# Kernel tuning notes

Measured on AMD Instinct MI355X. Metric: run time of the kernel, lower is better.

The kernel has to match this reference:

```python
import jax, jax.numpy as jnp
import numpy as np

B, S, D = 8, 2048, 768

def setup_inputs() -> dict:
    key = jax.random.key(0)
    k1, k2, k3, k4 = jax.random.split(key, 4)
    scale = 1.0 / np.sqrt(D)
    x = jax.random.normal(k1, (B, S, D), dtype=jnp.float32)
    W = jax.random.normal(k2, (D, D), dtype=jnp.float32) * scale
    proj_w = jax.random.normal(k3, (D, D), dtype=jnp.float32) * scale
    proj_b = jax.random.normal(k4, (D,), dtype=jnp.float32) * scale
    return {"x": x, "W": W, "proj_w": proj_w, "proj_b": proj_b}


def reference(x, W, proj_w, proj_b):
    # Wx = Linear(x) with torch convention: x @ W.T  -> [B,S,D]
    Wx = jnp.einsum('bsd,ed->bse', x, W)
    # s = Wx @ x^T  -> [B,S,S]
    s = jnp.einsum('bse,bte->bst', Wx, x)
    # mask diagonal (self) with -inf
    eye = jnp.eye(S, dtype=bool)
    s = jnp.where(eye[None, :, :], -jnp.inf, s)
    a = jax.nn.softmax(s, axis=2)
    # c = a @ x -> [B,S,D]
    c = jnp.einsum('bst,btd->bsd', a, x)
    # proj + relu, residual; dropout with p=0 is identity
    c = jax.nn.relu(jnp.einsum('bsd,ed->bse', c, proj_w) + proj_b)
    return x + c
```

## Files before the change

kernel.cpp:

```cpp
#include <hip/hip_runtime.h>
#include <hip/hip_bf16.h>

typedef _Float16 fp16_t;
typedef __attribute__((ext_vector_type(8))) _Float16 fp16x8;
typedef __attribute__((ext_vector_type(4))) _Float16 fp16x4;
typedef __attribute__((ext_vector_type(4))) float fx4;

#define GLDS(g, l)                                                              \
  __builtin_amdgcn_global_load_lds(                                             \
      (const __attribute__((address_space(1))) void*)(g),                       \
      (__attribute__((address_space(3))) void*)(l), 16, 0, 0)

enum { EPI_F32 = 0, EPI_F16 = 1, EPI_FUSE = 2, EPI_SOFT = 3 };

__device__ __forceinline__ void xcd_decode(int& bx, int& by, int& bz) {
  const int nx = gridDim.x, ny = gridDim.y;
  const int lid = (int)(blockIdx.x + nx * (blockIdx.y + ny * blockIdx.z));
  const int j = lid & 7, k = lid >> 3;
  bx = k % nx;
  const int s = j + 8 * (k / nx);
  by = s % ny;
  bz = s / ny;
}

template <bool ASPLIT, int EPI>
__global__ __launch_bounds__(256) void gemm_bt(
    const fp16_t* __restrict__ A1, const fp16_t* __restrict__ A2,
    const fp16_t* __restrict__ B1, void* __restrict__ Cv, int K, int lda,
    int ldb, long long sA, long long sB, long long sC,
    const float* __restrict__ bias, const float* __restrict__ resid,
    float* __restrict__ m_out, float* __restrict__ l_out) {
  constexpr int ALO = ASPLIT ? 128 * 32 : 0;
  __shared__ __align__(16) fp16_t As[128 * 32 + ALO];
  __shared__ __align__(16) fp16_t Bs[128 * 32];
  __shared__ float sred[(EPI == EPI_SOFT) ? 256 : 1];
  __shared__ float sfin[(EPI == EPI_SOFT) ? 128 : 1];

  const int tid  = threadIdx.x;
  const int lane = tid & 63;
  const int w    = tid >> 6;
  const int wr   = w >> 1;
  const int wc   = w & 1;

  int bx, by, bz;
  xcd_decode(bx, by, bz);
  const int N = (int)gridDim.x * 128;
  const long long tile_m = (long long)by * 128;
  const long long tile_n = (long long)bx * 128;
  const long long z = bz;
  const long long aoff = z * sA + tile_m * (long long)lda;
  const long long boff = z * sB + tile_n * (long long)ldb;

  fx4 acc[4][4];
#pragma unroll
  for (int i = 0; i < 4; i++)
#pragma unroll
    for (int j = 0; j < 4; j++) acc[i][j] = (fx4){0.f, 0.f, 0.f, 0.f};

  const int r_l = lane >> 2;
  const int c_l = ((((lane & 3) + ((r_l >> 1) & 3)) & 3) << 3);
  const int frow = lane & 15;
  const int qoff = (((lane >> 4) - ((frow >> 1) & 3)) & 3) << 3;

  const size_t sa0 = (size_t)(w * 16 + r_l) * lda + c_l;
  const size_t sa1 = (size_t)(64 + w * 16 + r_l) * lda + c_l;
  const size_t sb0 = (size_t)(w * 16 + r_l) * ldb + c_l;
  const size_t sb1 = (size_t)(64 + w * 16 + r_l) * ldb + c_l;
  const int ld0 = (w * 16) * 32;
  const int ld1 = (64 + w * 16) * 32;

  for (int kt = 0; kt < K; kt += 32) {
    __syncthreads();
    {
      const fp16_t* gah = A1 + aoff + kt;
      const fp16_t* gbh = B1 + boff + kt;
      GLDS(gah + sa0, &As[ld0]);
      GLDS(gah + sa1, &As[ld1]);
      GLDS(gbh + sb0, &Bs[ld0]);
      GLDS(gbh + sb1, &Bs[ld1]);
      if (ASPLIT) {
        const fp16_t* gal = A2 + aoff + kt;
        GLDS(gal + sa0, &As[ALO + ld0]);
        GLDS(gal + sa1, &As[ALO + ld1]);
      }
    }
    __syncthreads();

    fp16x8 afh[4], bbh[4], afl[4];
#pragma unroll
    for (int mi = 0; mi < 4; mi++)
      afh[mi] = *(const fp16x8*)&As[(wr * 64 + mi * 16 + frow) * 32 + qoff];
#pragma unroll
    for (int ni = 0; ni < 4; ni++)
      bbh[ni] = *(const fp16x8*)&Bs[(wc * 64 + ni * 16 + frow) * 32 + qoff];
    if (ASPLIT) {
#pragma unroll
      for (int mi = 0; mi < 4; mi++)
        afl[mi] =
            *(const fp16x8*)&As[ALO + (wr * 64 + mi * 16 + frow) * 32 + qoff];
    }

#pragma unroll
    for (int mi = 0; mi < 4; mi++)
#pragma unroll
      for (int ni = 0; ni < 4; ni++) {
        fx4 a = acc[mi][ni];
        a = __builtin_amdgcn_mfma_f32_16x16x32_f16(afh[mi], bbh[ni], a, 0, 0, 0);
        if (ASPLIT)
          a = __builtin_amdgcn_mfma_f32_16x16x32_f16(afl[mi], bbh[ni], a, 0, 0, 0);
        acc[mi][ni] = a;
      }
  }

  const int er = (lane >> 4) * 4;
  const int ec = lane & 15;
  const long long crow = tile_m + wr * 64;
  const long long ccol = tile_n + wc * 64;

  if constexpr (EPI == EPI_SOFT) {
    float pm[4][4];
#pragma unroll
    for (int mi = 0; mi < 4; mi++)
#pragma unroll
      for (int j = 0; j < 4; j++) {
        const long long r = crow + mi * 16 + er + j;
        float mx = -1e30f;
#pragma unroll
        for (int ni = 0; ni < 4; ni++) {
          const long long cc = ccol + ni * 16 + ec;
          float v = acc[mi][ni][j];
          if (r == cc) v = -1e30f;
          acc[mi][ni][j] = v;
          mx = fmaxf(mx, v);
        }
        pm[mi][j] = mx;
      }
#pragma unroll
    for (int o = 1; o < 16; o <<= 1)
#pragma unroll
      for (int mi = 0; mi < 4; mi++)
#pragma unroll
        for (int j = 0; j < 4; j++)
          pm[mi][j] = fmaxf(pm[mi][j], __shfl_xor(pm[mi][j], o, 64));
    if (ec == 0) {
#pragma unroll
      for (int mi = 0; mi < 4; mi++)
#pragma unroll
        for (int j = 0; j < 4; j++)
          sred[wc * 128 + wr * 64 + mi * 16 + er + j] = pm[mi][j];
    }
    __syncthreads();
    if (tid < 128) sfin[tid] = fmaxf(sred[tid], sred[128 + tid]);
    __syncthreads();
    float ps[4][4];
#pragma unroll
    for (int mi = 0; mi < 4; mi++)
#pragma unroll
      for (int j = 0; j < 4; j++) {
        const float m = sfin[wr * 64 + mi * 16 + er + j];
        float s = 0.f;
#pragma unroll
        for (int ni = 0; ni < 4; ni++) {
          const float e = __expf(acc[mi][ni][j] - m);
          acc[mi][ni][j] = e;
          s += e;
        }
        ps[mi][j] = s;
      }
#pragma unroll
    for (int o = 1; o < 16; o <<= 1)
#pragma unroll
      for (int mi = 0; mi < 4; mi++)
#pragma unroll
        for (int j = 0; j < 4; j++)
          ps[mi][j] += __shfl_xor(ps[mi][j], o, 64);
    __syncthreads();
    if (ec == 0) {
#pragma unroll
      for (int mi = 0; mi < 4; mi++)
#pragma unroll
        for (int j = 0; j < 4; j++)
          sred[wc * 128 + wr * 64 + mi * 16 + er + j] = ps[mi][j];
    }
    __syncthreads();
    if (tid < 128) {
      const long long si = (z * 16 + bx) * 2048 + tile_m + tid;
      m_out[si] = sfin[tid];
      l_out[si] = sred[tid] + sred[128 + tid];
    }
#pragma unroll
    for (int mi = 0; mi < 4; mi++)
#pragma unroll
      for (int j = 0; j < 4; j++) {
        const long long r = crow + mi * 16 + er + j;
#pragma unroll
        for (int ni = 0; ni < 4; ni++) {
          const long long cc = ccol + ni * 16 + ec;
          ((fp16_t*)Cv)[z * sC + r * N + cc] = (fp16_t)acc[mi][ni][j];
        }
      }
  } else {
#pragma unroll
    for (int mi = 0; mi < 4; mi++)
#pragma unroll
      for (int j = 0; j < 4; j++) {
        const long long r = crow + mi * 16 + er + j;
#pragma unroll
        for (int ni = 0; ni < 4; ni++) {
          const long long cc = ccol + ni * 16 + ec;
          const long long idx = z * sC + r * N + cc;
          const float v = acc[mi][ni][j];
          if (EPI == EPI_F32) {
            ((float*)Cv)[idx] = v;
          } else if (EPI == EPI_F16) {
            ((fp16_t*)Cv)[idx] = (fp16_t)v;
          } else {
            float u = v + bias[cc];
            u = u > 0.f ? u : 0.f;
            ((float*)Cv)[idx] = resid[r * N + cc] + u;
          }
        }
      }
  }
}

__global__ __launch_bounds__(256) void softmerge(
    const float* __restrict__ mstat, const float* __restrict__ lstat,
    float* __restrict__ scale) {
  const int gr = blockIdx.x * 256 + threadIdx.x;
  const int z = gr >> 11, row = gr & 2047;
  const long long base = ((long long)z * 16) * 2048 + row;
  float mv[16], lv[16];
  float m = -1e30f;
#pragma unroll
  for (int t = 0; t < 16; t++) {
    mv[t] = mstat[base + t * 2048];
    m = fmaxf(m, mv[t]);
  }
  float l = 0.f;
#pragma unroll
  for (int t = 0; t < 16; t++) {
    lv[t] = lstat[base + t * 2048];
    l += lv[t] * __expf(mv[t] - m);
  }
  const float il = 1.0f / l;
#pragma unroll
  for (int t = 0; t < 16; t++) scale[base + t * 2048] = __expf(mv[t] - m) * il;
}

__global__ __launch_bounds__(256) void gemm_pv(
    const fp16_t* __restrict__ P, const float* __restrict__ scale,
    const fp16_t* __restrict__ Bx, fp16_t* __restrict__ C) {
  __shared__ __align__(16) fp16_t As[128 * 32];
  __shared__ __align__(16) fp16_t Bs[128 * 32];

  const int tid  = threadIdx.x;
  const int lane = tid & 63;
  const int w    = tid >> 6;
  const int wr   = w >> 1;
  const int wc   = w & 1;

  int bx, by, bz;
  xcd_decode(bx, by, bz);
  const long long tile_m = (long long)by * 128;
  const long long tile_n = (long long)bx * 128;
  const long long z = bz;

  fx4 acc[4][4];
#pragma unroll
  for (int i = 0; i < 4; i++)
#pragma unroll
    for (int j = 0; j < 4; j++) acc[i][j] = (fx4){0.f, 0.f, 0.f, 0.f};

  const int r_l = lane >> 2;
  const int c_l = ((((lane & 3) + ((r_l >> 1) & 3)) & 3) << 3);
  const int frow = lane & 15;
  const int qoff = (((lane >> 4) - ((frow >> 1) & 3)) & 3) << 3;
  const size_t sb0 = (size_t)(w * 16 + r_l) * 2048 + c_l;
  const size_t sb1 = (size_t)(64 + w * 16 + r_l) * 2048 + c_l;
  const int ld0 = (w * 16) * 32;
  const int ld1 = (64 + w * 16) * 32;
  const fp16_t* B = Bx + z * (768LL * 2048) + tile_n * 2048;

  const int r = tid >> 1, hh = tid & 1;
  const int gm = (int)tile_m + r;
  const fp16_t* prow = P + z * (2048LL * 2048) + (long long)gm * 2048 + hh * 16;
  const float* srow = scale + (long long)z * 16 * 2048 + gm;
  const int slot0 = ((2 * hh + 0) - ((r >> 1) & 3)) & 3;
  const int slot1 = ((2 * hh + 1) - ((r >> 1) & 3)) & 3;
  fp16_t* const wp0 = &As[r * 32 + slot0 * 8];
  fp16_t* const wp1 = &As[r * 32 + slot1 * 8];

  for (int kt0 = 0; kt0 < 2048; kt0 += 128) {
    const fp16_t sh = (fp16_t)srow[(kt0 >> 7) * 2048];
#pragma unroll
    for (int ki = 0; ki < 4; ki++) {
      const int kt = kt0 + ki * 32;
      fp16x8 c0 = *(const fp16x8*)(prow + kt);
      fp16x8 c1 = *(const fp16x8*)(prow + kt + 8);
      c0 *= sh;
      c1 *= sh;
      __syncthreads();
      *(fp16x8*)wp0 = c0;
      *(fp16x8*)wp1 = c1;
      GLDS(B + kt + sb0, &Bs[ld0]);
      GLDS(B + kt + sb1, &Bs[ld1]);
      __syncthreads();

      fp16x8 af[4], bb[4];
#pragma unroll
      for (int mi = 0; mi < 4; mi++)
        af[mi] = *(const fp16x8*)&As[(wr * 64 + mi * 16 + frow) * 32 + qoff];
#pragma unroll
      for (int ni = 0; ni < 4; ni++)
        bb[ni] = *(const fp16x8*)&Bs[(wc * 64 + ni * 16 + frow) * 32 + qoff];
#pragma unroll
      for (int mi = 0; mi < 4; mi++)
#pragma unroll
        for (int ni = 0; ni < 4; ni++)
          acc[mi][ni] = __builtin_amdgcn_mfma_f32_16x16x32_f16(
              af[mi], bb[ni], acc[mi][ni], 0, 0, 0);
    }
  }

  const int er = (lane >> 4) * 4;
  const int ec = lane & 15;
  const long long crow = tile_m + wr * 64;
  const long long ccol = tile_n + wc * 64;
  fp16_t* Cz = C + z * (2048LL * 768);
#pragma unroll
  for (int mi = 0; mi < 4; mi++)
#pragma unroll
    for (int j = 0; j < 4; j++) {
      const long long rr = crow + mi * 16 + er + j;
#pragma unroll
      for (int ni = 0; ni < 4; ni++)
        Cz[rr * 768 + ccol + ni * 16 + ec] = (fp16_t)acc[mi][ni][j];
    }
}

__global__ __launch_bounds__(256) void prep_x(
    const float* __restrict__ x, fp16_t* __restrict__ xh,
    fp16_t* __restrict__ xl, fp16_t* __restrict__ xT) {
  __shared__ fp16_t t[32][33];
  const int b = blockIdx.z;
  const int d0 = blockIdx.x * 32;
  const int s0 = blockIdx.y * 32;
  const float* ib = x + (long long)b * 2048 * 768;
  const int tx = threadIdx.x & 31;
  const int ty = threadIdx.x >> 5;
#pragma unroll
  for (int i = 0; i < 4; i++) {
    const int srow = s0 + ty + i * 8;
    const long long idx = (long long)b * 2048 * 768 + (long long)srow * 768 + d0 + tx;
    const float v = ib[(long long)srow * 768 + d0 + tx];
    const fp16_t h = (fp16_t)v;
    xh[idx] = h;
    xl[idx] = (fp16_t)(v - (float)h);
    t[ty + i * 8][tx] = h;
  }
  __syncthreads();
#pragma unroll
  for (int i = 0; i < 4; i++)
    xT[(long long)b * 768 * 2048 + (long long)(d0 + ty + i * 8) * 2048 + s0 + tx] =
        t[tx][ty + i * 8];
}

__global__ __launch_bounds__(256) void cast_f32_f16(
    const float* __restrict__ in, fp16_t* __restrict__ out, int n4) {
  const int i = blockIdx.x * 256 + threadIdx.x;
  if (i >= n4) return;
  const float4 v = ((const float4*)in)[i];
  ((fp16x4*)out)[i] =
      (fp16x4){(fp16_t)v.x, (fp16_t)v.y, (fp16_t)v.z, (fp16_t)v.w};
}

extern "C" void kernel_launch(void* const* d_in, const int* in_sizes, int n_in,
                              void* d_out, int out_size, void* d_ws,
                              size_t ws_size, hipStream_t stream) {
  const float* x  = (const float*)d_in[0];
  const float* W  = (const float*)d_in[1];
  const float* pw = (const float*)d_in[2];
  const float* pb = (const float*)d_in[3];

  const long long S = 2048, D = 768;
  const long long BS = 8 * S;

  char* p = (char*)d_ws;
  auto carve = [&](long long bytes) {
    char* q = p;
    p += (bytes + 255) & ~255LL;
    return q;
  };
  fp16_t* xh = (fp16_t*)carve(BS * D * 2);
  fp16_t* xl = (fp16_t*)carve(BS * D * 2);
  fp16_t* xT = (fp16_t*)carve(BS * D * 2);
  fp16_t* Wx = (fp16_t*)carve(BS * D * 2);
  fp16_t* Wh = (fp16_t*)carve(D * D * 2);
  fp16_t* ph = (fp16_t*)carve(D * D * 2);
  float*  mstat = (float*)carve(BS * 16 * 4);
  float*  lstat = (float*)carve(BS * 16 * 4);
  float*  scale = (float*)carve(BS * 16 * 4);
  fp16_t* Ps = (fp16_t*)carve(8 * S * S * 2);
  fp16_t* cb = Wx;

  prep_x<<<dim3(24, 64, 8), 256, 0, stream>>>(x, xh, xl, xT);
  cast_f32_f16<<<(unsigned)(D * D / 4 / 256), 256, 0, stream>>>(
      W, Wh, (int)(D * D / 4));
  cast_f32_f16<<<(unsigned)(D * D / 4 / 256), 256, 0, stream>>>(
      pw, ph, (int)(D * D / 4));

  gemm_bt<true, EPI_F16><<<dim3(6, 128, 1), 256, 0, stream>>>(
      xh, xl, Wh, Wx, 768, 768, 768, 0, 0, 0, nullptr, nullptr, nullptr,
      nullptr);

  gemm_bt<false, EPI_SOFT><<<dim3(16, 16, 8), 256, 0, stream>>>(
      Wx, nullptr, xh, Ps, 768, 768, 768, S * D, S * D, S * S, nullptr,
      nullptr, mstat, lstat);

  softmerge<<<(unsigned)(BS / 256), 256, 0, stream>>>(mstat, lstat, scale);

  gemm_pv<<<dim3(6, 16, 8), 256, 0, stream>>>(Ps, scale, xT, cb);

  gemm_bt<false, EPI_FUSE><<<dim3(6, 128, 1), 256, 0, stream>>>(
      cb, nullptr, ph, (float*)d_out, 768, 768, 768, 0, 0, 0, pb, x, nullptr,
      nullptr);
}
```

Baseline: 404.4 us.

## Fuse softmax merge into PV gemm, double K step, merge weight casts

Removes the separate softmerge kernel by computing the per-tile softmax rescale factors inside gemm_pv's prologue, and merges the two weight-cast kernels into a single launch. Both GEMM kernels now stage 64 K-elements per barrier pair (two 32-wide LDS buffers) instead of 32, which halves the number of syncs. The softmax epilogue is also simplified: per-row shuffle reductions, one fewer barrier, and the exp values are written out directly. The aim is fewer launches and less synchronisation, at the cost of more LDS per block and redundant scale recomputation across the column blocks of gemm_pv.

```diff
diff --git a/kernel.cpp b/kernel.cpp
--- a/kernel.cpp
+++ b/kernel.cpp
@@ -31,10 +31,10 @@
     const float* __restrict__ bias, const float* __restrict__ resid,
     float* __restrict__ m_out, float* __restrict__ l_out) {
   constexpr int ALO = ASPLIT ? 128 * 32 : 0;
-  __shared__ __align__(16) fp16_t As[128 * 32 + ALO];
-  __shared__ __align__(16) fp16_t Bs[128 * 32];
-  __shared__ float sred[(EPI == EPI_SOFT) ? 256 : 1];
-  __shared__ float sfin[(EPI == EPI_SOFT) ? 128 : 1];
+  __shared__ __align__(16) fp16_t As[2][128 * 32 + ALO];
+  __shared__ __align__(16) fp16_t Bs[2][128 * 32];
+  __shared__ float smax[(EPI == EPI_SOFT) ? 256 : 1];
+  __shared__ float ssum[(EPI == EPI_SOFT) ? 256 : 1];
 
   const int tid  = threadIdx.x;
   const int lane = tid & 63;
@@ -69,47 +69,50 @@
   const int ld0 = (w * 16) * 32;
   const int ld1 = (64 + w * 16) * 32;
 
-  for (int kt = 0; kt < K; kt += 32) {
+  for (int kt = 0; kt < K; kt += 64) {
     __syncthreads();
-    {
-      const fp16_t* gah = A1 + aoff + kt;
-      const fp16_t* gbh = B1 + boff + kt;
-      GLDS(gah + sa0, &As[ld0]);
-      GLDS(gah + sa1, &As[ld1]);
-      GLDS(gbh + sb0, &Bs[ld0]);
-      GLDS(gbh + sb1, &Bs[ld1]);
+#pragma unroll
+    for (int h = 0; h < 2; h++) {
+      const fp16_t* gah = A1 + aoff + kt + h * 32;
+      const fp16_t* gbh = B1 + boff + kt + h * 32;
+      GLDS(gah + sa0, &As[h][ld0]);
+      GLDS(gah + sa1, &As[h][ld1]);
+      GLDS(gbh + sb0, &Bs[h][ld0]);
+      GLDS(gbh + sb1, &Bs[h][ld1]);
       if (ASPLIT) {
-        const fp16_t* gal = A2 + aoff + kt;
-        GLDS(gal + sa0, &As[ALO + ld0]);
-        GLDS(gal + sa1, &As[ALO + ld1]);
+        const fp16_t* gal = A2 + aoff + kt + h * 32;
+        GLDS(gal + sa0, &As[h][ALO + ld0]);
+        GLDS(gal + sa1, &As[h][ALO + ld1]);
       }
     }
     __syncthreads();
 
-    fp16x8 afh[4], bbh[4], afl[4];
-#pragma unroll
-    for (int mi = 0; mi < 4; mi++)
-      afh[mi] = *(const fp16x8*)&As[(wr * 64 + mi * 16 + frow) * 32 + qoff];
-#pragma unroll
-    for (int ni = 0; ni < 4; ni++)
-      bbh[ni] = *(const fp16x8*)&Bs[(wc * 64 + ni * 16 + frow) * 32 + qoff];
-    if (ASPLIT) {
+#pragma unroll
+    for (int h = 0; h < 2; h++) {
+      fp16x8 afh[4], bbh[4], afl[4];
 #pragma unroll
       for (int mi = 0; mi < 4; mi++)
-        afl[mi] =
-            *(const fp16x8*)&As[ALO + (wr * 64 + mi * 16 + frow) * 32 + qoff];
-    }
-
-#pragma unroll
-    for (int mi = 0; mi < 4; mi++)
-#pragma unroll
-      for (int ni = 0; ni < 4; ni++) {
-        fx4 a = acc[mi][ni];
-        a = __builtin_amdgcn_mfma_f32_16x16x32_f16(afh[mi], bbh[ni], a, 0, 0, 0);
-        if (ASPLIT)
-          a = __builtin_amdgcn_mfma_f32_16x16x32_f16(afl[mi], bbh[ni], a, 0, 0, 0);
-        acc[mi][ni] = a;
-      }
+        afh[mi] = *(const fp16x8*)&As[h][(wr * 64 + mi * 16 + frow) * 32 + qoff];
+#pragma unroll
+      for (int ni = 0; ni < 4; ni++)
+        bbh[ni] = *(const fp16x8*)&Bs[h][(wc * 64 + ni * 16 + frow) * 32 + qoff];
+      if (ASPLIT) {
+#pragma unroll
+        for (int mi = 0; mi < 4; mi++)
+          afl[mi] =
+              *(const fp16x8*)&As[h][ALO + (wr * 64 + mi * 16 + frow) * 32 + qoff];
+      }
+#pragma unroll
+      for (int mi = 0; mi < 4; mi++)
+#pragma unroll
+        for (int ni = 0; ni < 4; ni++) {
+          fx4 a = acc[mi][ni];
+          a = __builtin_amdgcn_mfma_f32_16x16x32_f16(afh[mi], bbh[ni], a, 0, 0, 0);
+          if (ASPLIT)
+            a = __builtin_amdgcn_mfma_f32_16x16x32_f16(afl[mi], bbh[ni], a, 0, 0, 0);
+          acc[mi][ni] = a;
+        }
+    }
   }
 
   const int er = (lane >> 4) * 4;
@@ -118,7 +121,6 @@
   const long long ccol = tile_n + wc * 64;
 
   if constexpr (EPI == EPI_SOFT) {
-    float pm[4][4];
 #pragma unroll
     for (int mi = 0; mi < 4; mi++)
 #pragma unroll
@@ -133,72 +135,35 @@
           acc[mi][ni][j] = v;
           mx = fmaxf(mx, v);
         }
-        pm[mi][j] = mx;
-      }
-#pragma unroll
-    for (int o = 1; o < 16; o <<= 1)
-#pragma unroll
-      for (int mi = 0; mi < 4; mi++)
-#pragma unroll
-        for (int j = 0; j < 4; j++)
-          pm[mi][j] = fmaxf(pm[mi][j], __shfl_xor(pm[mi][j], o, 64));
-    if (ec == 0) {
-#pragma unroll
-      for (int mi = 0; mi < 4; mi++)
-#pragma unroll
-        for (int j = 0; j < 4; j++)
-          sred[wc * 128 + wr * 64 + mi * 16 + er + j] = pm[mi][j];
-    }
+#pragma unroll
+        for (int o = 1; o < 16; o <<= 1) mx = fmaxf(mx, __shfl_xor(mx, o, 64));
+        if (ec == 0) smax[wc * 128 + wr * 64 + mi * 16 + er + j] = mx;
+      }
     __syncthreads();
-    if (tid < 128) sfin[tid] = fmaxf(sred[tid], sred[128 + tid]);
-    __syncthreads();
-    float ps[4][4];
 #pragma unroll
     for (int mi = 0; mi < 4; mi++)
 #pragma unroll
       for (int j = 0; j < 4; j++) {
-        const float m = sfin[wr * 64 + mi * 16 + er + j];
+        const int rid = wr * 64 + mi * 16 + er + j;
+        const float m = fmaxf(smax[rid], smax[128 + rid]);
+        const long long r = crow + mi * 16 + er + j;
         float s = 0.f;
 #pragma unroll
         for (int ni = 0; ni < 4; ni++) {
           const float e = __expf(acc[mi][ni][j] - m);
-          acc[mi][ni][j] = e;
           s += e;
+          ((fp16_t*)Cv)[z * sC + r * N + (ccol + ni * 16 + ec)] = (fp16_t)e;
         }
-        ps[mi][j] = s;
-      }
-#pragma unroll
-    for (int o = 1; o < 16; o <<= 1)
-#pragma unroll
-      for (int mi = 0; mi < 4; mi++)
-#pragma unroll
-        for (int j = 0; j < 4; j++)
-          ps[mi][j] += __shfl_xor(ps[mi][j], o, 64);
-    __syncthreads();
-    if (ec == 0) {
-#pragma unroll
-      for (int mi = 0; mi < 4; mi++)
-#pragma unroll
-        for (int j = 0; j < 4; j++)
-          sred[wc * 128 + wr * 64 + mi * 16 + er + j] = ps[mi][j];
-    }
+#pragma unroll
+        for (int o = 1; o < 16; o <<= 1) s += __shfl_xor(s, o, 64);
+        if (ec == 0) ssum[wc * 128 + rid] = s;
+      }
     __syncthreads();
     if (tid < 128) {
       const long long si = (z * 16 + bx) * 2048 + tile_m + tid;
-      m_out[si] = sfin[tid];
-      l_out[si] = sred[tid] + sred[128 + tid];
-    }
-#pragma unroll
-    for (int mi = 0; mi < 4; mi++)
-#pragma unroll
-      for (int j = 0; j < 4; j++) {
-        const long long r = crow + mi * 16 + er + j;
-#pragma unroll
-        for (int ni = 0; ni < 4; ni++) {
-          const long long cc = ccol + ni * 16 + ec;
-          ((fp16_t*)Cv)[z * sC + r * N + cc] = (fp16_t)acc[mi][ni][j];
-        }
-      }
+      m_out[si] = fmaxf(smax[tid], smax[128 + tid]);
+      l_out[si] = ssum[tid] + ssum[128 + tid];
+    }
   } else {
 #pragma unroll
     for (int mi = 0; mi < 4; mi++)
@@ -224,35 +189,13 @@
   }
 }
 
-__global__ __launch_bounds__(256) void softmerge(
-    const float* __restrict__ mstat, const float* __restrict__ lstat,
-    float* __restrict__ scale) {
-  const int gr = blockIdx.x * 256 + threadIdx.x;
-  const int z = gr >> 11, row = gr & 2047;
-  const long long base = ((long long)z * 16) * 2048 + row;
-  float mv[16], lv[16];
-  float m = -1e30f;
-#pragma unroll
-  for (int t = 0; t < 16; t++) {
-    mv[t] = mstat[base + t * 2048];
-    m = fmaxf(m, mv[t]);
-  }
-  float l = 0.f;
-#pragma unroll
-  for (int t = 0; t < 16; t++) {
-    lv[t] = lstat[base + t * 2048];
-    l += lv[t] * __expf(mv[t] - m);
-  }
-  const float il = 1.0f / l;
-#pragma unroll
-  for (int t = 0; t < 16; t++) scale[base + t * 2048] = __expf(mv[t] - m) * il;
-}
-
 __global__ __launch_bounds__(256) void gemm_pv(
-    const fp16_t* __restrict__ P, const float* __restrict__ scale,
-    const fp16_t* __restrict__ Bx, fp16_t* __restrict__ C) {
-  __shared__ __align__(16) fp16_t As[128 * 32];
-  __shared__ __align__(16) fp16_t Bs[128 * 32];
+    const fp16_t* __restrict__ P, const float* __restrict__ mstat,
+    const float* __restrict__ lstat, const fp16_t* __restrict__ Bx,
+    fp16_t* __restrict__ C) {
+  __shared__ __align__(16) fp16_t As[2][128 * 32];
+  __shared__ __align__(16) fp16_t Bs[2][128 * 32];
+  __shared__ float sc[16][128];
 
   const int tid  = threadIdx.x;
   const int lane = tid & 63;
@@ -265,6 +208,23 @@
   const long long tile_m = (long long)by * 128;
   const long long tile_n = (long long)bx * 128;
   const long long z = bz;
+
+  if (tid < 128) {
+    const long long base = z * 16 * 2048 + tile_m + tid;
+    float mv[16];
+    float m = -1e30f;
+#pragma unroll
+    for (int t = 0; t < 16; t++) {
+      mv[t] = mstat[base + t * 2048];
+      m = fmaxf(m, mv[t]);
+    }
+    float l = 0.f;
+#pragma unroll
+    for (int t = 0; t < 16; t++) l += lstat[base + t * 2048] * __expf(mv[t] - m);
+    const float il = 1.0f / l;
+#pragma unroll
+    for (int t = 0; t < 16; t++) sc[t][tid] = __expf(mv[t] - m) * il;
+  }
 
   fx4 acc[4][4];
 #pragma unroll
@@ -285,41 +245,52 @@
   const int r = tid >> 1, hh = tid & 1;
   const int gm = (int)tile_m + r;
   const fp16_t* prow = P + z * (2048LL * 2048) + (long long)gm * 2048 + hh * 16;
-  const float* srow = scale + (long long)z * 16 * 2048 + gm;
   const int slot0 = ((2 * hh + 0) - ((r >> 1) & 3)) & 3;
   const int slot1 = ((2 * hh + 1) - ((r >> 1) & 3)) & 3;
-  fp16_t* const wp0 = &As[r * 32 + slot0 * 8];
-  fp16_t* const wp1 = &As[r * 32 + slot1 * 8];
+  const int wp0 = r * 32 + slot0 * 8;
+  const int wp1 = r * 32 + slot1 * 8;
+
+  __syncthreads();
 
   for (int kt0 = 0; kt0 < 2048; kt0 += 128) {
-    const fp16_t sh = (fp16_t)srow[(kt0 >> 7) * 2048];
-#pragma unroll
-    for (int ki = 0; ki < 4; ki++) {
-      const int kt = kt0 + ki * 32;
-      fp16x8 c0 = *(const fp16x8*)(prow + kt);
-      fp16x8 c1 = *(const fp16x8*)(prow + kt + 8);
-      c0 *= sh;
-      c1 *= sh;
+    const fp16_t sh = (fp16_t)sc[kt0 >> 7][r];
+#pragma unroll
+    for (int kk = 0; kk < 2; kk++) {
+      const int kt = kt0 + kk * 64;
+      fp16x8 v0[2], v1[2];
+#pragma unroll
+      for (int h = 0; h < 2; h++) {
+        v0[h] = *(const fp16x8*)(prow + kt + h * 32);
+        v1[h] = *(const fp16x8*)(prow + kt + h * 32 + 8);
+        v0[h] *= sh;
+        v1[h] *= sh;
+      }
       __syncthreads();
-      *(fp16x8*)wp0 = c0;
-      *(fp16x8*)wp1 = c1;
-      GLDS(B + kt + sb0, &Bs[ld0]);
-      GLDS(B + kt + sb1, &Bs[ld1]);
+#pragma unroll
+      for (int h = 0; h < 2; h++) {
+        *(fp16x8*)&As[h][wp0] = v0[h];
+        *(fp16x8*)&As[h][wp1] = v1[h];
+        GLDS(B + kt + h * 32 + sb0, &Bs[h][ld0]);
+        GLDS(B + kt + h * 32 + sb1, &Bs[h][ld1]);
+      }
       __syncthreads();
 
-      fp16x8 af[4], bb[4];
-#pragma unroll
-      for (int mi = 0; mi < 4; mi++)
-        af[mi] = *(const fp16x8*)&As[(wr * 64 + mi * 16 + frow) * 32 + qoff];
-#pragma unroll
-      for (int ni = 0; ni < 4; ni++)
-        bb[ni] = *(const fp16x8*)&Bs[(wc * 64 + ni * 16 + frow) * 32 + qoff];
-#pragma unroll
-      for (int mi = 0; mi < 4; mi++)
+#pragma unroll
+      for (int h = 0; h < 2; h++) {
+        fp16x8 af[4], bb[4];
+#pragma unroll
+        for (int mi = 0; mi < 4; mi++)
+          af[mi] = *(const fp16x8*)&As[h][(wr * 64 + mi * 16 + frow) * 32 + qoff];
 #pragma unroll
         for (int ni = 0; ni < 4; ni++)
-          acc[mi][ni] = __builtin_amdgcn_mfma_f32_16x16x32_f16(
-              af[mi], bb[ni], acc[mi][ni], 0, 0, 0);
+          bb[ni] = *(const fp16x8*)&Bs[h][(wc * 64 + ni * 16 + frow) * 32 + qoff];
+#pragma unroll
+        for (int mi = 0; mi < 4; mi++)
+#pragma unroll
+          for (int ni = 0; ni < 4; ni++)
+            acc[mi][ni] = __builtin_amdgcn_mfma_f32_16x16x32_f16(
+                af[mi], bb[ni], acc[mi][ni], 0, 0, 0);
+      }
     }
   }
 
@@ -366,10 +337,13 @@
         t[tx][ty + i * 8];
 }
 
-__global__ __launch_bounds__(256) void cast_f32_f16(
-    const float* __restrict__ in, fp16_t* __restrict__ out, int n4) {
+__global__ __launch_bounds__(256) void cast2_f32_f16(
+    const float* __restrict__ a, const float* __restrict__ b,
+    fp16_t* __restrict__ oa, fp16_t* __restrict__ ob, int n4) {
   const int i = blockIdx.x * 256 + threadIdx.x;
   if (i >= n4) return;
+  const float* in = blockIdx.y == 0 ? a : b;
+  fp16_t* out = blockIdx.y == 0 ? oa : ob;
   const float4 v = ((const float4*)in)[i];
   ((fp16x4*)out)[i] =
       (fp16x4){(fp16_t)v.x, (fp16_t)v.y, (fp16_t)v.z, (fp16_t)v.w};
@@ -400,15 +374,12 @@
   fp16_t* ph = (fp16_t*)carve(D * D * 2);
   float*  mstat = (float*)carve(BS * 16 * 4);
   float*  lstat = (float*)carve(BS * 16 * 4);
-  float*  scale = (float*)carve(BS * 16 * 4);
   fp16_t* Ps = (fp16_t*)carve(8 * S * S * 2);
   fp16_t* cb = Wx;
 
   prep_x<<<dim3(24, 64, 8), 256, 0, stream>>>(x, xh, xl, xT);
-  cast_f32_f16<<<(unsigned)(D * D / 4 / 256), 256, 0, stream>>>(
-      W, Wh, (int)(D * D / 4));
-  cast_f32_f16<<<(unsigned)(D * D / 4 / 256), 256, 0, stream>>>(
-      pw, ph, (int)(D * D / 4));
+  cast2_f32_f16<<<dim3((unsigned)(D * D / 4 / 256), 2), 256, 0, stream>>>(
+      W, pw, Wh, ph, (int)(D * D / 4));
 
   gemm_bt<true, EPI_F16><<<dim3(6, 128, 1), 256, 0, stream>>>(
       xh, xl, Wh, Wx, 768, 768, 768, 0, 0, 0, nullptr, nullptr, nullptr,
@@ -418,9 +389,7 @@
       Wx, nullptr, xh, Ps, 768, 768, 768, S * D, S * D, S * S, nullptr,
       nullptr, mstat, lstat);
 
-  softmerge<<<(unsigned)(BS / 256), 256, 0, stream>>>(mstat, lstat, scale);
-
-  gemm_pv<<<dim3(6, 16, 8), 256, 0, stream>>>(Ps, scale, xT, cb);
+  gemm_pv<<<dim3(6, 16, 8), 256, 0, stream>>>(Ps, mstat, lstat, xT, cb);
 
   gemm_bt<false, EPI_FUSE><<<dim3(6, 128, 1), 256, 0, stream>>>(
       cb, nullptr, ph, (float*)d_out, 768, 768, 768, 0, 0, 0, pb, x, nullptr,
```

Measured after the change: 380.1 us. -6.0%, faster.
